# Kernel optimization log

Hardware: AMD Instinct MI355X
Metric: run time of the kernel (lower is better)

Reference implementation:

```python
import jax, jax.numpy as jnp
import numpy as np

N, D, V = 16384, 2048, 8192  # rows, code bits, val_range (codebook size)


def setup_inputs() -> dict:
    key = jax.random.key(0)
    k1, k2 = jax.random.split(key)
    x = jax.random.normal(k1, (N, D), dtype=jnp.float32)   # encoded rows
    di = jax.random.normal(k2, (D, V), dtype=jnp.float32)  # decode codebook (fwd.di)
    return {"x": x, "di": di}


def reference(x, di):
    # Original loops over rows doing (1,D)@(D,V) then argmax; batched this is one
    # GEMM [N,D]@[D,V] -> [N,V] followed by argmax over the V axis, cast to float32
    # (the torch code stores the index into a float32 output tensor).
    scores = jnp.matmul(x, di)                  # [N, V]
    return jnp.argmax(scores, axis=1).astype(jnp.float32)  # [N]
```

## Files before the change

kernel.cpp:

```cpp
#include <hip/hip_runtime.h>

typedef _Float16 f16x8 __attribute__((ext_vector_type(8)));
typedef float f32x4 __attribute__((ext_vector_type(4)));
typedef float f32x16 __attribute__((ext_vector_type(16)));
typedef int i32x4 __attribute__((ext_vector_type(4)));
typedef int i32x8 __attribute__((ext_vector_type(8)));

__device__ __forceinline__ unsigned int fkey(float f) {
    unsigned int u = __float_as_uint(f);
    return u ^ ((u & 0x80000000u) ? 0xFFFFFFFFu : 0x80000000u);
}
__device__ __forceinline__ float unkey(unsigned int k) {
    unsigned int u = (k & 0x80000000u) ? (k ^ 0x80000000u) : ~k;
    return __uint_as_float(u);
}

__device__ __forceinline__ unsigned int f32_to_e4m3(float f) {
    float a = fabsf(f);
    a = fminf(a, 448.0f);
    unsigned int s = (__float_as_uint(f) >> 24) & 0x80u;
    if (a < 0.015625f) {
        int m = (int)rintf(a * 512.0f);
        return s | (unsigned int)m;
    }
    int e = ilogbf(a);
    float step = ldexpf(1.0f, e - 3);
    int q = (int)rintf(a / step);
    if (q == 16) { e += 1; q = 8; }
    return s | (unsigned int)(((e + 7) << 3) | (q - 8));
}

__global__ __launch_bounds__(256) void prep_x_q(
    const float* __restrict__ x, unsigned char* __restrict__ Xq)
{
    size_t base = ((size_t)blockIdx.x * 256 + threadIdx.x) * 8;
    float4 a0 = *(const float4*)(x + base);
    float4 a1 = *(const float4*)(x + base + 4);
    float v[8] = {a0.x, a0.y, a0.z, a0.w, a1.x, a1.y, a1.z, a1.w};
    unsigned long long b = 0;
#pragma unroll
    for (int j = 0; j < 8; ++j)
        b |= (unsigned long long)f32_to_e4m3(v[j]) << (8 * j);
    *(unsigned long long*)(Xq + base) = b;
}

__global__ __launch_bounds__(256) void prep_di_q(
    const float* __restrict__ di, unsigned char* __restrict__ DqT,
    _Float16* __restrict__ DhT, _Float16* __restrict__ DlT, int D, int V)
{
    int v  = blockIdx.x * 64 + (threadIdx.x & 63);
    int d0 = blockIdx.y * 32 + (threadIdx.x >> 6) * 8;
    f16x8 h, l;
    unsigned long long b = 0;
#pragma unroll
    for (int j = 0; j < 8; ++j) {
        float val = di[(size_t)(d0 + j) * V + v];
        _Float16 hh = (_Float16)val;
        h[j] = hh;
        l[j] = (_Float16)(val - (float)hh);
        b |= (unsigned long long)f32_to_e4m3(val) << (8 * j);
    }
    *(unsigned long long*)(DqT + (size_t)v * D + d0) = b;
    *(f16x8*)(DhT + (size_t)v * D + d0) = h;
    *(f16x8*)(DlT + (size_t)v * D + d0) = l;
}

__global__ __launch_bounds__(256, 2) void gemm_mx_top2(
    const unsigned char* __restrict__ Xq, const unsigned char* __restrict__ DqT,
    unsigned long long* __restrict__ cand, int N, int D, int V)
{
    __shared__ __align__(16) unsigned char sm[49152];

    const int tid = threadIdx.x;
    const int w = tid >> 6, lane = tid & 63;
    const int l31 = lane & 31, hl = lane >> 5;

    const int cpx = gridDim.x >> 3;
    const int swz = (blockIdx.x & 7) * cpx + (blockIdx.x >> 3);
    const int bm = (swz >> 5) * 128;
    const int bn = (swz & 31) * 256;

    const int srow_in = lane >> 2;
    const int sp      = lane & 3;
    auto stage = [&](int buf, int k0) {
#pragma unroll
        for (int i = 0; i < 6; ++i) {
            const int c = w * 6 + i;
            const int isB = (c >= 8);
            const int cc = isB ? c - 8 : c;
            const int row = cc * 16 + srow_in;
            const int slog = sp ^ ((row >> 1) & 3);
            const unsigned char* src =
                (isB ? DqT + (size_t)(bn + row) * D : Xq + (size_t)(bm + row) * D)
                + k0 + slog * 16;
            __builtin_amdgcn_global_load_lds(
                (const __attribute__((address_space(1))) void*)src,
                (__attribute__((address_space(3))) void*)
                    (sm + buf * 24576 + (isB ? 8192 : 0) + cc * 1024),
                16, 0, 0);
        }
    };
    auto ldfrag = [&](int buf, int op, int r) -> i32x8 {
        const unsigned char* base =
            sm + buf * 24576 + (op ? 8192 : 0) + (r >> 4) * 1024 + (r & 15) * 64;
        const int sw = (r >> 1) & 3;
        i32x4 lo = *(const i32x4*)(base + (((hl << 1)    ) ^ sw) * 16);
        i32x4 hi = *(const i32x4*)(base + (((hl << 1) | 1) ^ sw) * 16);
        return __builtin_shufflevector(lo, hi, 0, 1, 2, 3, 4, 5, 6, 7);
    };

    f32x16 acc[4][2];
#pragma unroll
    for (int fm = 0; fm < 4; ++fm)
#pragma unroll
        for (int fn = 0; fn < 2; ++fn)
#pragma unroll
            for (int q = 0; q < 16; ++q) acc[fm][fn][q] = 0.0f;

    const int nt = D / 64;
    int cb = 0;

    stage(0, 0);
    __syncthreads();

#pragma unroll 1
    for (int t = 0; t < nt; ++t) {
        if (t + 1 < nt) stage(cb ^ 1, (t + 1) * 64);

        i32x8 b0 = ldfrag(cb, 1, w * 64 + l31);
        i32x8 b1 = ldfrag(cb, 1, w * 64 + 32 + l31);
#pragma unroll
        for (int fm = 0; fm < 4; ++fm) {
            i32x8 a = ldfrag(cb, 0, fm * 32 + l31);
            acc[fm][0] = __builtin_amdgcn_mfma_scale_f32_32x32x64_f8f6f4(
                a, b0, acc[fm][0], 0, 0, 0, 0x7F7F7F7F, 0, 0x7F7F7F7F);
            acc[fm][1] = __builtin_amdgcn_mfma_scale_f32_32x32x64_f8f6f4(
                a, b1, acc[fm][1], 0, 0, 0, 0x7F7F7F7F, 0, 0x7F7F7F7F);
        }
        __syncthreads();
        cb ^= 1;
    }

    const int nblk = V >> 8;
    const int blkn = bn >> 8;
#pragma unroll
    for (int fm = 0; fm < 4; ++fm)
#pragma unroll
        for (int j = 0; j < 16; ++j) {
            const int row = bm + fm * 32 + (j & 3) + 8 * (j >> 2) + 4 * hl;
            const int c0 = bn + w * 64 + l31;
            unsigned long long p0 =
                ((unsigned long long)fkey(acc[fm][0][j]) << 32) |
                (unsigned long long)(0xFFFFFFFFu - (unsigned int)c0);
            unsigned long long p1 =
                ((unsigned long long)fkey(acc[fm][1][j]) << 32) |
                (unsigned long long)(0xFFFFFFFFu - (unsigned int)(c0 + 32));
            unsigned long long t1 = p0 > p1 ? p0 : p1;
            unsigned long long t2 = p0 > p1 ? p1 : p0;
#pragma unroll
            for (int m = 1; m < 32; m <<= 1) {
                unsigned long long o1 = __shfl_xor(t1, m);
                unsigned long long o2 = __shfl_xor(t2, m);
                unsigned long long n1 = t1 > o1 ? t1 : o1;
                unsigned long long lo = t1 > o1 ? o1 : t1;
                unsigned long long m2 = t2 > o2 ? t2 : o2;
                t2 = lo > m2 ? lo : m2;
                t1 = n1;
            }
            if (l31 == 0) {
                size_t ci = (((size_t)row * nblk + blkn) * 4 + w) * 2;
                cand[ci] = t1;
                cand[ci + 1] = t2;
            }
        }
}

#define DELTA 16.5f

__global__ __launch_bounds__(256) void refine_kernel(
    const unsigned long long* __restrict__ cand,
    const float* __restrict__ X,
    const _Float16* __restrict__ DhT, const _Float16* __restrict__ DlT,
    float* __restrict__ out, int N, int D, int V)
{
    const int w = threadIdx.x >> 6, lane = threadIdx.x & 63;
    const int r = blockIdx.x * 4 + w;
    if (r >= N) return;

    const int nent = (V >> 8) * 8;
    const unsigned long long* cr = cand + (size_t)r * nent;

    unsigned long long p[4];
#pragma unroll
    for (int i = 0; i < 4; ++i) p[i] = cr[lane * 4 + i];

    unsigned long long pmax = p[0];
#pragma unroll
    for (int i = 1; i < 4; ++i) if (p[i] > pmax) pmax = p[i];
#pragma unroll
    for (int m = 1; m < 64; m <<= 1) {
        unsigned long long o = __shfl_xor(pmax, m);
        if (o > pmax) pmax = o;
    }

    const float s1 = unkey((unsigned int)(pmax >> 32));
    const unsigned int kthr = fkey(s1 - DELTA);

    int cnt = 0;
    unsigned long long masks[4];
#pragma unroll
    for (int i = 0; i < 4; ++i) {
        masks[i] = __ballot((unsigned int)(p[i] >> 32) >= kthr);
        cnt += __popcll(masks[i]);
    }

    if (cnt <= 1) {
        if (lane == 0)
            out[r] = (float)(0xFFFFFFFFu - (unsigned int)(pmax & 0xFFFFFFFFull));
        return;
    }

    const float* xrow = X + (size_t)r * D;
    float xbuf[32];
#pragma unroll
    for (int q = 0; q < 8; ++q) {
        float4 xv = *(const float4*)(xrow + lane * 32 + q * 4);
        xbuf[q * 4 + 0] = xv.x; xbuf[q * 4 + 1] = xv.y;
        xbuf[q * 4 + 2] = xv.z; xbuf[q * 4 + 3] = xv.w;
    }

    unsigned long long bestp = 0;
    for (int i = 0; i < 4; ++i) {
        unsigned long long mask = masks[i];
        while (mask) {
            const int src = __ffsll((unsigned long long)mask) - 1;
            mask &= mask - 1;
            const unsigned long long cp = __shfl(p[i], src);
            const int col = (int)(0xFFFFFFFFu - (unsigned int)(cp & 0xFFFFFFFFull));

            const f16x8* dh = (const f16x8*)(DhT + (size_t)col * D) + lane * 4;
            const f16x8* dl = (const f16x8*)(DlT + (size_t)col * D) + lane * 4;
            float s = 0.0f;
#pragma unroll
            for (int q = 0; q < 4; ++q) {
                f16x8 h = dh[q], l = dl[q];
#pragma unroll
                for (int e = 0; e < 8; ++e)
                    s = fmaf(xbuf[q * 8 + e], (float)h[e] + (float)l[e], s);
            }
#pragma unroll
            for (int m = 1; m < 64; m <<= 1) s += __shfl_xor(s, m);

            const unsigned long long pp =
                ((unsigned long long)fkey(s) << 32) |
                (unsigned long long)(0xFFFFFFFFu - (unsigned int)col);
            if (pp > bestp) bestp = pp;
        }
    }
    if (lane == 0)
        out[r] = (float)(0xFFFFFFFFu - (unsigned int)(bestp & 0xFFFFFFFFull));
}

#define FBK 16
#define FTM 8
#define FTN 8

__global__ __launch_bounds__(256) void gemm_argmax_fp32_kernel(
    const float* __restrict__ A, const float* __restrict__ B,
    unsigned long long* __restrict__ best, int N, int D, int V)
{
    __shared__ float As[FBK][128 + 4];
    __shared__ float Bs[FBK][128 + 4];

    const int tid = threadIdx.x;
    const int tx = tid & 15;
    const int ty = tid >> 4;
    const int bm = blockIdx.y * 128;
    const int bn = blockIdx.x * 128;

    const int arow  = tid >> 2;
    const int acol4 = tid & 3;
    const int brow  = tid >> 5;
    const int bcol4 = tid & 31;

    float acc[FTM][FTN];
#pragma unroll
    for (int i = 0; i < FTM; ++i)
#pragma unroll
        for (int j = 0; j < FTN; ++j) acc[i][j] = 0.0f;

    for (int k0 = 0; k0 < D; k0 += FBK) {
        float4 a0 = *reinterpret_cast<const float4*>(&A[(size_t)(bm + arow) * D + k0 + acol4 * 4]);
        float4 a1 = *reinterpret_cast<const float4*>(&A[(size_t)(bm + arow + 64) * D + k0 + acol4 * 4]);
        float4 b0 = *reinterpret_cast<const float4*>(&B[(size_t)(k0 + brow) * V + bn + bcol4 * 4]);
        float4 b1 = *reinterpret_cast<const float4*>(&B[(size_t)(k0 + brow + 8) * V + bn + bcol4 * 4]);

        As[acol4 * 4 + 0][arow] = a0.x;
        As[acol4 * 4 + 1][arow] = a0.y;
        As[acol4 * 4 + 2][arow] = a0.z;
        As[acol4 * 4 + 3][arow] = a0.w;
        As[acol4 * 4 + 0][arow + 64] = a1.x;
        As[acol4 * 4 + 1][arow + 64] = a1.y;
        As[acol4 * 4 + 2][arow + 64] = a1.z;
        As[acol4 * 4 + 3][arow + 64] = a1.w;
        *reinterpret_cast<float4*>(&Bs[brow][bcol4 * 4]) = b0;
        *reinterpret_cast<float4*>(&Bs[brow + 8][bcol4 * 4]) = b1;

        __syncthreads();
#pragma unroll
        for (int kk = 0; kk < FBK; ++kk) {
            float4 av0 = *reinterpret_cast<const float4*>(&As[kk][ty * FTM]);
            float4 av1 = *reinterpret_cast<const float4*>(&As[kk][ty * FTM + 4]);
            float4 bv0 = *reinterpret_cast<const float4*>(&Bs[kk][tx * FTN]);
            float4 bv1 = *reinterpret_cast<const float4*>(&Bs[kk][tx * FTN + 4]);
            float a[FTM] = {av0.x, av0.y, av0.z, av0.w, av1.x, av1.y, av1.z, av1.w};
            float b[FTN] = {bv0.x, bv0.y, bv0.z, bv0.w, bv1.x, bv1.y, bv1.z, bv1.w};
#pragma unroll
            for (int i = 0; i < FTM; ++i)
#pragma unroll
                for (int j = 0; j < FTN; ++j)
                    acc[i][j] = fmaf(a[i], b[j], acc[i][j]);
        }
        __syncthreads();
    }

#pragma unroll
    for (int i = 0; i < FTM; ++i) {
        float bv = acc[i][0];
        int bc = bn + tx * FTN;
#pragma unroll
        for (int j = 1; j < FTN; ++j) {
            float v = acc[i][j];
            int c = bn + tx * FTN + j;
            if (v > bv) { bv = v; bc = c; }
        }
        unsigned long long packed =
            ((unsigned long long)fkey(bv) << 32) |
            (unsigned long long)(0xFFFFFFFFu - (unsigned int)bc);
#pragma unroll
        for (int m = 1; m < 16; m <<= 1) {
            unsigned long long o = __shfl_xor(packed, m, 16);
            if (o > packed) packed = o;
        }
        if (tx == 0) atomicMax(&best[bm + ty * FTM + i], packed);
    }
}

__global__ void decode_kernel(const unsigned long long* __restrict__ best,
                              float* __restrict__ out, int N)
{
    int i = blockIdx.x * blockDim.x + threadIdx.x;
    if (i < N) {
        unsigned int inv = (unsigned int)(best[i] & 0xFFFFFFFFull);
        out[i] = (float)(0xFFFFFFFFu - inv);
    }
}

extern "C" void kernel_launch(void* const* d_in, const int* in_sizes, int n_in,
                              void* d_out, int out_size, void* d_ws, size_t ws_size,
                              hipStream_t stream) {
    const float* A = (const float*)d_in[0];
    const float* B = (const float*)d_in[1];
    float* out = (float*)d_out;

    const int N = out_size;
    const int D = in_sizes[0] / N;
    const int V = in_sizes[1] / D;

    const size_t szXq = (size_t)N * D;
    const size_t szDq = (size_t)D * V;
    const size_t szDh = (size_t)D * V * sizeof(_Float16);
    const size_t candsz = (size_t)N * (V / 256) * 4 * 2 * 8;
    const size_t need = szXq + szDq + 2 * szDh + candsz;

    if (ws_size >= need) {
        char* wsp = (char*)d_ws;
        unsigned char* Xq  = (unsigned char*)(wsp);
        unsigned char* DqT = (unsigned char*)(wsp + szXq);
        _Float16* DhT = (_Float16*)(wsp + szXq + szDq);
        _Float16* DlT = (_Float16*)(wsp + szXq + szDq + szDh);
        unsigned long long* cand =
            (unsigned long long*)(wsp + szXq + szDq + 2 * szDh);

        prep_x_q<<<(int)(((size_t)N * D) / (256 * 8)), 256, 0, stream>>>(A, Xq);
        prep_di_q<<<dim3(V / 64, D / 32), 256, 0, stream>>>(B, DqT, DhT, DlT, D, V);
        gemm_mx_top2<<<(N / 128) * (V / 256), 256, 0, stream>>>(
            Xq, DqT, cand, N, D, V);
        refine_kernel<<<(N + 3) / 4, 256, 0, stream>>>(
            cand, A, DhT, DlT, out, N, D, V);
    } else {
        unsigned long long* best = (unsigned long long*)d_ws;
        hipMemsetAsync(best, 0, (size_t)N * sizeof(unsigned long long), stream);
        gemm_argmax_fp32_kernel<<<dim3(V / 128, N / 128), 256, 0, stream>>>(A, B, best, N, D, V);
        decode_kernel<<<(N + 255) / 256, 256, 0, stream>>>(best, out, N);
    }
}
```

Measured before the change: 723.1 us.

## Triple-buffer LDS staging with explicit vmcnt waits in FP8 GEMM

Moves the FP8 MFMA GEMM from double to triple buffering in shared memory, prefetching two K-tiles ahead. The single __syncthreads is replaced by a partial s_waitcnt vmcnt followed by a raw s_barrier, so loads for later tiles stay in flight while the current tile is computed. Per-thread source and destination offsets are hoisted out of the staging lambda. LDS per block grows to 72KB, which may lower occupancy under launch_bounds(256,2), and the hand-counted vmcnt values have to match the number of loads issued.

After: 713.5 us. Within noise of the previous version (-1.3%).

```diff
diff --git a/kernel.cpp b/kernel.cpp
--- a/kernel.cpp
+++ b/kernel.cpp
@@ -69,7 +69,7 @@
     const unsigned char* __restrict__ Xq, const unsigned char* __restrict__ DqT,
     unsigned long long* __restrict__ cand, int N, int D, int V)
 {
-    __shared__ __align__(16) unsigned char sm[49152];
+    __shared__ __align__(16) unsigned char sm[73728];
 
     const int tid = threadIdx.x;
     const int w = tid >> 6, lane = tid & 63;
@@ -82,21 +82,28 @@
 
     const int srow_in = lane >> 2;
     const int sp      = lane & 3;
+
+    const unsigned char* srcbase[6];
+    int dstoff[6];
+#pragma unroll
+    for (int i = 0; i < 6; ++i) {
+        const int c = w * 6 + i;
+        const int isB = (c >= 8);
+        const int cc = isB ? c - 8 : c;
+        const int row = cc * 16 + srow_in;
+        const int slog = sp ^ ((row >> 1) & 3);
+        srcbase[i] = (isB ? DqT + (size_t)(bn + row) * D
+                          : Xq + (size_t)(bm + row) * D) + slog * 16;
+        dstoff[i] = (isB ? 8192 : 0) + cc * 1024;
+    }
+
     auto stage = [&](int buf, int k0) {
 #pragma unroll
         for (int i = 0; i < 6; ++i) {
-            const int c = w * 6 + i;
-            const int isB = (c >= 8);
-            const int cc = isB ? c - 8 : c;
-            const int row = cc * 16 + srow_in;
-            const int slog = sp ^ ((row >> 1) & 3);
-            const unsigned char* src =
-                (isB ? DqT + (size_t)(bn + row) * D : Xq + (size_t)(bm + row) * D)
-                + k0 + slog * 16;
             __builtin_amdgcn_global_load_lds(
-                (const __attribute__((address_space(1))) void*)src,
+                (const __attribute__((address_space(1))) void*)(srcbase[i] + k0),
                 (__attribute__((address_space(3))) void*)
-                    (sm + buf * 24576 + (isB ? 8192 : 0) + cc * 1024),
+                    (sm + buf * 24576 + dstoff[i]),
                 16, 0, 0);
         }
     };
@@ -119,13 +126,22 @@
 
     const int nt = D / 64;
     int cb = 0;
+    int sb = 2;
 
     stage(0, 0);
-    __syncthreads();
+    stage(1, 64);
 
 #pragma unroll 1
     for (int t = 0; t < nt; ++t) {
-        if (t + 1 < nt) stage(cb ^ 1, (t + 1) * 64);
+        if (t + 2 < nt) {
+            stage(sb, (t + 2) * 64);
+            asm volatile("s_waitcnt vmcnt(12)" ::: "memory");
+        } else if (t + 1 < nt) {
+            asm volatile("s_waitcnt vmcnt(6)" ::: "memory");
+        } else {
+            asm volatile("s_waitcnt vmcnt(0)" ::: "memory");
+        }
+        __builtin_amdgcn_s_barrier();
 
         i32x8 b0 = ldfrag(cb, 1, w * 64 + l31);
         i32x8 b1 = ldfrag(cb, 1, w * 64 + 32 + l31);
@@ -137,8 +153,12 @@
             acc[fm][1] = __builtin_amdgcn_mfma_scale_f32_32x32x64_f8f6f4(
                 a, b1, acc[fm][1], 0, 0, 0, 0x7F7F7F7F, 0, 0x7F7F7F7F);
         }
-        __syncthreads();
-        cb ^= 1;
+
+        asm volatile("s_waitcnt lgkmcnt(0)" ::: "memory");
+        __builtin_amdgcn_s_barrier();
+
+        cb = (cb == 2) ? 0 : cb + 1;
+        sb = (sb == 2) ? 0 : sb + 1;
     }
 
     const int nblk = V >> 8;
```

## Shrink GEMM block tile to 128x128 with 2x2 warp layout for higher occupancy

Applied to the files above, without the earlier changes.

The FP8 MFMA GEMM block tile shrinks from 128x256 to 128x128, and the four waves are arranged 2x2, each computing a 64x64 sub-tile instead of 128x64. LDS use drops to 32 KB and launch bounds ask for 4 blocks per CU, trading per-block operand reuse for more resident waves and latency hiding. Staging source addresses are precomputed once outside the K loop. Candidate layout changes to 128 column groups per row (256 entries), which is hardcoded in the refine kernel and so assumes V=8192.

Measured after the change: 658.5 us. 8.9% less time.

```diff
diff --git a/kernel.cpp b/kernel.cpp
--- a/kernel.cpp
+++ b/kernel.cpp
@@ -65,53 +65,61 @@
     *(f16x8*)(DlT + (size_t)v * D + d0) = l;
 }
 
-__global__ __launch_bounds__(256, 2) void gemm_mx_top2(
+__global__ __launch_bounds__(256, 4) void gemm_mx_top2(
     const unsigned char* __restrict__ Xq, const unsigned char* __restrict__ DqT,
     unsigned long long* __restrict__ cand, int N, int D, int V)
 {
-    __shared__ __align__(16) unsigned char sm[49152];
+    __shared__ __align__(16) unsigned char sm[32768];
 
     const int tid = threadIdx.x;
     const int w = tid >> 6, lane = tid & 63;
+    const int wr = w >> 1, wc = w & 1;
     const int l31 = lane & 31, hl = lane >> 5;
 
     const int cpx = gridDim.x >> 3;
     const int swz = (blockIdx.x & 7) * cpx + (blockIdx.x >> 3);
-    const int bm = (swz >> 5) * 128;
-    const int bn = (swz & 31) * 256;
+    const int bm = (swz >> 6) * 128;
+    const int bn = (swz & 63) * 128;
 
     const int srow_in = lane >> 2;
     const int sp      = lane & 3;
+
+    const unsigned char* srcbase[4];
+    int dstoff[4];
+#pragma unroll
+    for (int i = 0; i < 4; ++i) {
+        const int c = w * 4 + i;
+        const int isB = (c >= 8);
+        const int cc = isB ? c - 8 : c;
+        const int row = cc * 16 + srow_in;
+        const int slog = sp ^ ((row >> 1) & 3);
+        srcbase[i] = (isB ? DqT + (size_t)(bn + row) * D
+                          : Xq + (size_t)(bm + row) * D) + slog * 16;
+        dstoff[i] = (isB ? 8192 : 0) + cc * 1024;
+    }
+
     auto stage = [&](int buf, int k0) {
 #pragma unroll
-        for (int i = 0; i < 6; ++i) {
-            const int c = w * 6 + i;
-            const int isB = (c >= 8);
-            const int cc = isB ? c - 8 : c;
-            const int row = cc * 16 + srow_in;
-            const int slog = sp ^ ((row >> 1) & 3);
-            const unsigned char* src =
-                (isB ? DqT + (size_t)(bn + row) * D : Xq + (size_t)(bm + row) * D)
-                + k0 + slog * 16;
+        for (int i = 0; i < 4; ++i) {
             __builtin_amdgcn_global_load_lds(
-                (const __attribute__((address_space(1))) void*)src,
+                (const __attribute__((address_space(1))) void*)(srcbase[i] + k0),
                 (__attribute__((address_space(3))) void*)
-                    (sm + buf * 24576 + (isB ? 8192 : 0) + cc * 1024),
+                    (sm + buf * 16384 + dstoff[i]),
                 16, 0, 0);
         }
     };
     auto ldfrag = [&](int buf, int op, int r) -> i32x8 {
         const unsigned char* base =
-            sm + buf * 24576 + (op ? 8192 : 0) + (r >> 4) * 1024 + (r & 15) * 64;
+            sm + buf * 16384 + (op ? 8192 : 0) + (r >> 4) * 1024 + (r & 15) * 64;
         const int sw = (r >> 1) & 3;
         i32x4 lo = *(const i32x4*)(base + (((hl << 1)    ) ^ sw) * 16);
         i32x4 hi = *(const i32x4*)(base + (((hl << 1) | 1) ^ sw) * 16);
         return __builtin_shufflevector(lo, hi, 0, 1, 2, 3, 4, 5, 6, 7);
     };
 
-    f32x16 acc[4][2];
-#pragma unroll
-    for (int fm = 0; fm < 4; ++fm)
+    f32x16 acc[2][2];
+#pragma unroll
+    for (int fm = 0; fm < 2; ++fm)
 #pragma unroll
         for (int fn = 0; fn < 2; ++fn)
 #pragma unroll
@@ -127,28 +135,29 @@
     for (int t = 0; t < nt; ++t) {
         if (t + 1 < nt) stage(cb ^ 1, (t + 1) * 64);
 
-        i32x8 b0 = ldfrag(cb, 1, w * 64 + l31);
-        i32x8 b1 = ldfrag(cb, 1, w * 64 + 32 + l31);
-#pragma unroll
-        for (int fm = 0; fm < 4; ++fm) {
-            i32x8 a = ldfrag(cb, 0, fm * 32 + l31);
-            acc[fm][0] = __builtin_amdgcn_mfma_scale_f32_32x32x64_f8f6f4(
-                a, b0, acc[fm][0], 0, 0, 0, 0x7F7F7F7F, 0, 0x7F7F7F7F);
-            acc[fm][1] = __builtin_amdgcn_mfma_scale_f32_32x32x64_f8f6f4(
-                a, b1, acc[fm][1], 0, 0, 0, 0x7F7F7F7F, 0, 0x7F7F7F7F);
-        }
+        i32x8 b0 = ldfrag(cb, 1, wc * 64 + l31);
+        i32x8 b1 = ldfrag(cb, 1, wc * 64 + 32 + l31);
+        i32x8 a0 = ldfrag(cb, 0, wr * 64 + l31);
+        i32x8 a1 = ldfrag(cb, 0, wr * 64 + 32 + l31);
+        acc[0][0] = __builtin_amdgcn_mfma_scale_f32_32x32x64_f8f6f4(
+            a0, b0, acc[0][0], 0, 0, 0, 0x7F7F7F7F, 0, 0x7F7F7F7F);
+        acc[0][1] = __builtin_amdgcn_mfma_scale_f32_32x32x64_f8f6f4(
+            a0, b1, acc[0][1], 0, 0, 0, 0x7F7F7F7F, 0, 0x7F7F7F7F);
+        acc[1][0] = __builtin_amdgcn_mfma_scale_f32_32x32x64_f8f6f4(
+            a1, b0, acc[1][0], 0, 0, 0, 0x7F7F7F7F, 0, 0x7F7F7F7F);
+        acc[1][1] = __builtin_amdgcn_mfma_scale_f32_32x32x64_f8f6f4(
+            a1, b1, acc[1][1], 0, 0, 0, 0x7F7F7F7F, 0, 0x7F7F7F7F);
+
         __syncthreads();
         cb ^= 1;
     }
 
-    const int nblk = V >> 8;
-    const int blkn = bn >> 8;
-#pragma unroll
-    for (int fm = 0; fm < 4; ++fm)
+#pragma unroll
+    for (int fm = 0; fm < 2; ++fm)
 #pragma unroll
         for (int j = 0; j < 16; ++j) {
-            const int row = bm + fm * 32 + (j & 3) + 8 * (j >> 2) + 4 * hl;
-            const int c0 = bn + w * 64 + l31;
+            const int row = bm + wr * 64 + fm * 32 + (j & 3) + 8 * (j >> 2) + 4 * hl;
+            const int c0 = bn + wc * 64 + l31;
             unsigned long long p0 =
                 ((unsigned long long)fkey(acc[fm][0][j]) << 32) |
                 (unsigned long long)(0xFFFFFFFFu - (unsigned int)c0);
@@ -168,7 +177,7 @@
                 t1 = n1;
             }
             if (l31 == 0) {
-                size_t ci = (((size_t)row * nblk + blkn) * 4 + w) * 2;
+                size_t ci = ((size_t)row * 128 + (bn >> 6) + wc) * 2;
                 cand[ci] = t1;
                 cand[ci + 1] = t2;
             }
@@ -187,7 +196,7 @@
     const int r = blockIdx.x * 4 + w;
     if (r >= N) return;
 
-    const int nent = (V >> 8) * 8;
+    const int nent = 256;
     const unsigned long long* cr = cand + (size_t)r * nent;
 
     unsigned long long p[4];
@@ -370,7 +379,7 @@
     const size_t szXq = (size_t)N * D;
     const size_t szDq = (size_t)D * V;
     const size_t szDh = (size_t)D * V * sizeof(_Float16);
-    const size_t candsz = (size_t)N * (V / 256) * 4 * 2 * 8;
+    const size_t candsz = (size_t)N * 256 * 8;
     const size_t need = szXq + szDq + 2 * szDh + candsz;
 
     if (ws_size >= need) {
@@ -384,7 +393,7 @@
 
         prep_x_q<<<(int)(((size_t)N * D) / (256 * 8)), 256, 0, stream>>>(A, Xq);
         prep_di_q<<<dim3(V / 64, D / 32), 256, 0, stream>>>(B, DqT, DhT, DlT, D, V);
-        gemm_mx_top2<<<(N / 128) * (V / 256), 256, 0, stream>>>(
+        gemm_mx_top2<<<(N / 128) * (V / 128), 256, 0, stream>>>(
             Xq, DqT, cand, N, D, V);
         refine_kernel<<<(N + 3) / 4, 256, 0, stream>>>(
             cand, A, DhT, DlT, out, N, D, V);
```
